# Kernel tuning notes

Measured on AMD Instinct MI355X. Metric: run time of the kernel, lower is better.

## Reference

```python
import jax, jax.numpy as jnp
from jax import lax
import numpy as np

P = 32      # num_series
H = 128     # hidden units
B = 32      # batch
T = 256     # sequence length

def setup_inputs() -> dict:
    key = jax.random.key(0)
    ks = jax.random.split(key, 8)
    s = 1.0 / np.sqrt(H)
    X     = jax.random.normal(ks[0], (B, T, P), dtype=jnp.float32)
    # per-network LSTM weights, PyTorch gate order (i, f, g, o) stacked in 4H
    W_ih  = jax.random.uniform(ks[1], (P, 4 * H, P), dtype=jnp.float32, minval=-s, maxval=s)
    W_hh  = jax.random.uniform(ks[2], (P, 4 * H, H), dtype=jnp.float32, minval=-s, maxval=s)
    b_ih  = jax.random.uniform(ks[3], (P, 4 * H), dtype=jnp.float32, minval=-s, maxval=s)
    b_hh  = jax.random.uniform(ks[4], (P, 4 * H), dtype=jnp.float32, minval=-s, maxval=s)
    # Conv1d(hidden, 1, kernel_size=1) == per-timestep linear H -> 1, per network
    W_out = jax.random.uniform(ks[5], (P, H), dtype=jnp.float32, minval=-s, maxval=s)
    b_out = jax.random.uniform(ks[6], (P,), dtype=jnp.float32, minval=-s, maxval=s)
    return {"X": X, "W_ih": W_ih, "W_hh": W_hh, "b_ih": b_ih,
            "b_hh": b_hh, "W_out": W_out, "b_out": b_out}

def reference(X, W_ih, W_hh, b_ih, b_hh, W_out, b_out):
    # X: (B, T, P); p independent 1-layer LSTMs run on the same input,
    # batched along a network axis n (size P) with distinct weights.
    # Precompute input projections for all steps/networks: (T, B, P, 4H)
    xproj = jnp.einsum('btd,nkd->tbnk', X, W_ih) + b_ih + b_hh

    def step(carry, xp_t):
        h, c = carry                                   # (B, P, H) each
        gates = xp_t + jnp.einsum('bnh,nkh->bnk', h, W_hh)
        i, f, g, o = jnp.split(gates, 4, axis=-1)
        i = jax.nn.sigmoid(i)
        f = jax.nn.sigmoid(f)
        g = jnp.tanh(g)
        o = jax.nn.sigmoid(o)
        c = f * c + i * g
        h = o * jnp.tanh(c)
        return (h, c), h

    h0 = jnp.zeros((X.shape[0], W_ih.shape[0], W_hh.shape[2]), X.dtype)
    (_, _), hs = lax.scan(step, (h0, h0), xproj)        # hs: (T, B, P, H)
    # 1x1 conv head per network, then concat over networks -> (B, T, P)
    pred = jnp.einsum('tbnh,nh->btn', hs, W_out) + b_out
    return pred
```

## Files before the change

kernel.cpp:

```cpp
#include <hip/hip_runtime.h>
#include <stdint.h>

#define NP 32
#define NH 128
#define NB 32
#define NT 256
#define FH 512

typedef __attribute__((ext_vector_type(4))) float float4_t;
typedef __attribute__((ext_vector_type(8))) __bf16 bf16x8;
typedef __attribute__((ext_vector_type(4))) __bf16 bf16x4;

static __device__ __forceinline__ float4_t mfma_bf16(bf16x8 a, bf16x8 b, float4_t c) {
  return __builtin_amdgcn_mfma_f32_16x16x32_bf16(a, b, c, 0, 0, 0);
}

#define LOG2E 1.4426950408889634f

#define BAR() __asm__ volatile("s_waitcnt lgkmcnt(0)\n\ts_barrier" ::: "memory")


__global__ __launch_bounds__(512, 1) void xcvt(
    const float* __restrict__ X, __bf16* __restrict__ Xb)
{
  const int i = (blockIdx.x * 512 + threadIdx.x) * 4;
  float4_t v = *(const float4_t*)(X + i);
  bf16x4 o;
#pragma unroll
  for (int j = 0; j < 4; ++j) o[j] = (__bf16)v[j];
  *(bf16x4*)(Xb + i) = o;
}

__global__ __attribute__((amdgpu_flat_work_group_size(512, 512),
                          amdgpu_waves_per_eu(2, 2)))
void clstm_fused7(
    const __bf16* __restrict__ Xb, const float* __restrict__ Wih,
    const float* __restrict__ Whh, const float* __restrict__ bih,
    const float* __restrict__ bhh, const float* __restrict__ Wout,
    const float* __restrict__ bout, float* __restrict__ out)
{
  const int net = blockIdx.x & 31, bq = blockIdx.x >> 5;
  const int tid = threadIdx.x;
  const int w = tid >> 6, lane = tid & 63;
  const int quad = lane >> 4, l16 = lane & 15;

  __shared__ __bf16 hfrag[2][4][4][4][8];

  { ((int*)hfrag)[tid] = 0; }
  __syncthreads();

  bf16x8 bfrag[4][5];
  float4_t bias4[4];
#pragma unroll
  for (int g = 0; g < 4; ++g) {
    const float scale = (g == 2) ? (-2.0f*LOG2E) : (-LOG2E);
    const int col = g*NH + w*16 + l16;
#pragma unroll
    for (int kc = 0; kc < 5; ++kc) {
      const float* src = (kc == 0) ? (Wih + ((size_t)net*FH + col)*NP + quad*8)
                                   : (Whh + ((size_t)net*FH + col)*NH + (kc-1)*32 + quad*8);
      bf16x8 bf;
#pragma unroll
      for (int j = 0; j < 8; ++j) bf[j] = (__bf16)(src[j] * scale);
      bfrag[g][kc] = bf;
    }
    const float b = (bih[net*FH + col] + bhh[net*FH + col]) * scale;
    bias4[g] = (float4_t){b, b, b, b};
  }

  bf16x8 wof[4];
#pragma unroll
  for (int kc = 0; kc < 4; ++kc) {
    const float* wp = Wout + net*NH + kc*32 + quad*8;
#pragma unroll
    for (int j = 0; j < 8; ++j) wof[kc][j] = (__bf16)wp[j];
  }
  const float bo = bout[net];

  float cs = 0.f;
  const float S2 = -2.0f*LOG2E;

  int xoff = (bq*4 + (l16 >> 2))*(NT*NP) + quad*8;

  const int kcp = w >> 1, q2 = ((w & 1) << 1) | (l16 >> 3), jj = l16 & 7;

  float* outp = out + ((size_t)(bq*4 + quad))*(NT*NP) + net;

  bf16x8 ax = *(const bf16x8*)(Xb + xoff);
  xoff += NP;

#define STEP(RD, WR, T_)                                                      \
  do {                                                                        \
                 \
    bf16x8 ah0 = *(const bf16x8*)&hfrag[RD][0][quad][l16 >> 2][0];            \
    bf16x8 ah1 = *(const bf16x8*)&hfrag[RD][1][quad][l16 >> 2][0];            \
    bf16x8 ah2 = *(const bf16x8*)&hfrag[RD][2][quad][l16 >> 2][0];            \
    bf16x8 ah3 = *(const bf16x8*)&hfrag[RD][3][quad][l16 >> 2][0];            \
        \
    float4_t a0 = mfma_bf16(ax, bfrag[0][0], bias4[0]);                       \
    float4_t a1 = mfma_bf16(ax, bfrag[1][0], bias4[1]);                       \
    float4_t a2 = mfma_bf16(ax, bfrag[2][0], bias4[2]);                       \
    float4_t a3 = mfma_bf16(ax, bfrag[3][0], bias4[3]);                       \
               \
    if ((T_) + 1 < NT)                                                        \
      ax = *(const bf16x8*)(Xb + xoff);                                       \
    xoff += NP;                                                               \
                       \
    a0 = mfma_bf16(ah0, bfrag[0][1], a0);                                     \
    a1 = mfma_bf16(ah0, bfrag[1][1], a1);                                     \
    a2 = mfma_bf16(ah0, bfrag[2][1], a2);                                     \
    a3 = mfma_bf16(ah0, bfrag[3][1], a3);                                     \
    a0 = mfma_bf16(ah1, bfrag[0][2], a0);                                     \
    a1 = mfma_bf16(ah1, bfrag[1][2], a1);                                     \
    a2 = mfma_bf16(ah1, bfrag[2][2], a2);                                     \
    a3 = mfma_bf16(ah1, bfrag[3][2], a3);                                     \
    a0 = mfma_bf16(ah2, bfrag[0][3], a0);                                     \
    a1 = mfma_bf16(ah2, bfrag[1][3], a1);                                     \
    a2 = mfma_bf16(ah2, bfrag[2][3], a2);                                     \
    a3 = mfma_bf16(ah2, bfrag[3][3], a3);                                     \
    a0 = mfma_bf16(ah3, bfrag[0][4], a0);                                     \
    a1 = mfma_bf16(ah3, bfrag[1][4], a1);                                     \
    a2 = mfma_bf16(ah3, bfrag[2][4], a2);                                     \
    a3 = mfma_bf16(ah3, bfrag[3][4], a3);                                     \
                \
    float ei = __builtin_amdgcn_exp2f(a0[0]);                                 \
    float ig = __builtin_amdgcn_rcpf(1.0f + ei);              \
    float ef = __builtin_amdgcn_exp2f(a1[0]);                                 \
    float fg = __builtin_amdgcn_rcpf(1.0f + ef);              \
    float eg = __builtin_amdgcn_exp2f(fminf(a2[0], 126.0f));                  \
    float rg = __builtin_amdgcn_rcpf(1.0f + eg);                              \
    float t0 = S2 * rg;                                                       \
    float gg2 = t0 - t0 * eg;                                 \
    float eo = __builtin_amdgcn_exp2f(a3[0]);                                 \
    float og = __builtin_amdgcn_rcpf(1.0f + eo);              \
    cs = fg * cs + ig * gg2;                                      \
    float ec = __builtin_amdgcn_exp2f(fminf(cs, 126.0f));                     \
    float rc = __builtin_amdgcn_rcpf(1.0f + ec);                              \
    float h_ = og * (rc - ec * rc);                            \
                       \
    hfrag[WR][kcp][q2][quad][jj] = (__bf16)h_;                                \
          \
    if ((T_) > 0 && w == ((T_) & 7)) {                                        \
      float4_t p0 = {bo, bo, bo, bo};                                         \
      float4_t p1 = {0.f, 0.f, 0.f, 0.f};                                     \
      p0 = mfma_bf16(ah0, wof[0], p0);                                        \
      p1 = mfma_bf16(ah2, wof[2], p1);                                        \
      p0 = mfma_bf16(ah1, wof[1], p0);                                        \
      p1 = mfma_bf16(ah3, wof[3], p1);                                        \
      if (l16 == 0)                                                           \
        outp[(size_t)((T_) - 1)*NP] = p0[0] + p1[0];                          \
    }                                                                         \
    BAR();                                                                    \
  } while (0)

  for (int t = 0; t < NT; t += 2) {
    STEP(0, 1, t);
    STEP(1, 0, t + 1);
  }
#undef STEP

  if (w == 0) {
    bf16x8 ahf[4];
#pragma unroll
    for (int kc = 0; kc < 4; ++kc)
      ahf[kc] = *(const bf16x8*)&hfrag[NT & 1][kc][quad][l16 >> 2][0];
    float4_t p0 = {bo, bo, bo, bo};
    float4_t p1 = {0.f, 0.f, 0.f, 0.f};
    p0 = mfma_bf16(ahf[0], wof[0], p0);
    p1 = mfma_bf16(ahf[2], wof[2], p1);
    p0 = mfma_bf16(ahf[1], wof[1], p0);
    p1 = mfma_bf16(ahf[3], wof[3], p1);
    if (l16 == 0)
      outp[(size_t)(NT - 1)*NP] = p0[0] + p1[0];
  }
}

__global__ __launch_bounds__(512, 1) void clstm_fused_fb(
    const float* __restrict__ X, const float* __restrict__ Wih,
    const float* __restrict__ Whh, const float* __restrict__ bih,
    const float* __restrict__ bhh, const float* __restrict__ Wout,
    const float* __restrict__ bout, float* __restrict__ out)
{
  const int net = blockIdx.x >> 3, bq = blockIdx.x & 7;
  const int tid = threadIdx.x;
  const int w = tid >> 6, lane = tid & 63;
  const int quad = lane >> 4, l16 = lane & 15;

  __shared__ __bf16 hfrag[2][4][4][4][8];
  { ((int*)hfrag)[tid] = 0; }
  __syncthreads();

  bf16x8 bfrag[4][5];
  float4_t bias4[4];
#pragma unroll
  for (int g = 0; g < 4; ++g) {
    const float scale = (g == 2) ? (-2.0f*LOG2E) : (-LOG2E);
    const int col = g*NH + w*16 + l16;
#pragma unroll
    for (int kc = 0; kc < 5; ++kc) {
      const float* src = (kc == 0) ? (Wih + ((size_t)net*FH + col)*NP + quad*8)
                                   : (Whh + ((size_t)net*FH + col)*NH + (kc-1)*32 + quad*8);
      bf16x8 bf;
#pragma unroll
      for (int j = 0; j < 8; ++j) bf[j] = (__bf16)(src[j] * scale);
      bfrag[g][kc] = bf;
    }
    const float b = (bih[net*FH + col] + bhh[net*FH + col]) * scale;
    bias4[g] = (float4_t){b, b, b, b};
  }

  bf16x8 wof[4];
#pragma unroll
  for (int kc = 0; kc < 4; ++kc) {
    const float* wp = Wout + net*NH + kc*32 + quad*8;
#pragma unroll
    for (int j = 0; j < 8; ++j) wof[kc][j] = (__bf16)wp[j];
  }
  const float bo = bout[net];

  float cs = 0.f;
  const float S2 = -2.0f*LOG2E;

  const float* xrow = X + (size_t)(bq*4 + (l16 & 3))*(NT*NP) + quad*8;
  const int kcp = w >> 1, q2 = ((w & 1) << 1) | (l16 >> 3), jj = l16 & 7;
  float* outp = out + ((size_t)bq*4)*(NT*NP) + net;

  bf16x8 ax;
  {
    float xv0[8];
    *(float4_t*)&xv0[0] = *(const float4_t*)xrow;
    *(float4_t*)&xv0[4] = *(const float4_t*)(xrow + 4);
#pragma unroll
    for (int j = 0; j < 8; ++j) ax[j] = (__bf16)xv0[j];
  }
  const float* xp = xrow + NP;
  float xv[8] = {0.f,0.f,0.f,0.f,0.f,0.f,0.f,0.f};

  for (int t = 0; t < NT; ++t) {
    const int rd = t & 1, wr = rd ^ 1;
    bf16x8 ah[4];
#pragma unroll
    for (int kc = 0; kc < 4; ++kc)
      ah[kc] = *(const bf16x8*)&hfrag[rd][kc][quad][l16 & 3][0];
    float4_t accx[4];
#pragma unroll
    for (int g = 0; g < 4; ++g)
      accx[g] = mfma_bf16(ax, bfrag[g][0], bias4[g]);
    if (t + 1 < NT) {
      *(float4_t*)&xv[0] = *(const float4_t*)xp;
      *(float4_t*)&xv[4] = *(const float4_t*)(xp + 4);
    }
    float4_t acc[4];
#pragma unroll
    for (int g = 0; g < 4; ++g) {
      float4_t a0 = mfma_bf16(ah[0], bfrag[g][1], accx[g]);
      float4_t a1 = mfma_bf16(ah[2], bfrag[g][3], (float4_t){0.f,0.f,0.f,0.f});
      a0 = mfma_bf16(ah[1], bfrag[g][2], a0);
      a1 = mfma_bf16(ah[3], bfrag[g][4], a1);
      acc[g] = a0 + a1;
    }
    float gv[4];
#pragma unroll
    for (int g = 0; g < 4; ++g) {
      float a01 = (quad & 1) ? acc[g][1] : acc[g][0];
      float a23 = (quad & 1) ? acc[g][3] : acc[g][2];
      gv[g] = (quad & 2) ? a23 : a01;
    }
    float h;
    {
      float ei = __builtin_amdgcn_exp2f(gv[0]);
      float ig = __builtin_amdgcn_rcpf(1.0f + ei);
      float ef = __builtin_amdgcn_exp2f(gv[1]);
      float fg = __builtin_amdgcn_rcpf(1.0f + ef);
      float eg = __builtin_amdgcn_exp2f(fminf(gv[2], 126.0f));
      float rg = __builtin_amdgcn_rcpf(1.0f + eg);
      float t0 = S2 * rg;
      float gg2 = t0 - t0 * eg;
      float eo = __builtin_amdgcn_exp2f(gv[3]);
      float og = __builtin_amdgcn_rcpf(1.0f + eo);
      cs = fg * cs + ig * gg2;
      float ec = __builtin_amdgcn_exp2f(fminf(cs, 126.0f));
      float rc = __builtin_amdgcn_rcpf(1.0f + ec);
      float th = rc - ec * rc;
      h = og * th;
    }
    hfrag[wr][kcp][q2][quad][jj] = (__bf16)h;
    if (w == 0 && t > 0) {
      float4_t p0 = {bo, bo, bo, bo};
      float4_t p1 = {0.f, 0.f, 0.f, 0.f};
      p0 = mfma_bf16(ah[0], wof[0], p0);
      p1 = mfma_bf16(ah[2], wof[2], p1);
      p0 = mfma_bf16(ah[1], wof[1], p0);
      p1 = mfma_bf16(ah[3], wof[3], p1);
      float4_t po = p0 + p1;
      if (lane == 0) {
#pragma unroll
        for (int r = 0; r < 4; ++r)
          outp[(size_t)r*(NT*NP) + (t - 1)*NP] = po[r];
      }
    }
#pragma unroll
    for (int j = 0; j < 8; ++j) ax[j] = (__bf16)xv[j];
    xp += NP;
    BAR();
  }

  if (w == 0) {
    bf16x8 ahf[4];
#pragma unroll
    for (int kc = 0; kc < 4; ++kc)
      ahf[kc] = *(const bf16x8*)&hfrag[NT & 1][kc][quad][l16 & 3][0];
    float4_t p0 = {bo, bo, bo, bo};
    float4_t p1 = {0.f, 0.f, 0.f, 0.f};
    p0 = mfma_bf16(ahf[0], wof[0], p0);
    p1 = mfma_bf16(ahf[2], wof[2], p1);
    p0 = mfma_bf16(ahf[1], wof[1], p0);
    p1 = mfma_bf16(ahf[3], wof[3], p1);
    float4_t po = p0 + p1;
    if (lane == 0) {
#pragma unroll
      for (int r = 0; r < 4; ++r)
        outp[(size_t)r*(NT*NP) + (NT - 1)*NP] = po[r];
    }
  }
}

extern "C" void kernel_launch(void* const* d_in, const int* in_sizes, int n_in,
                              void* d_out, int out_size, void* d_ws, size_t ws_size,
                              hipStream_t stream) {
  const float* X    = (const float*)d_in[0];
  const float* Wih  = (const float*)d_in[1];
  const float* Whh  = (const float*)d_in[2];
  const float* bih  = (const float*)d_in[3];
  const float* bhh  = (const float*)d_in[4];
  const float* Wout = (const float*)d_in[5];
  const float* bout = (const float*)d_in[6];
  float* out = (float*)d_out;
  (void)in_sizes; (void)n_in; (void)out_size;

  const size_t need = (size_t)NB*NT*NP*2;
  if (d_ws != nullptr && ws_size >= need) {
    __bf16* wsX = (__bf16*)d_ws;
    xcvt<<<128, 512, 0, stream>>>(X, wsX);
    clstm_fused7<<<256, 512, 0, stream>>>(wsX, Wih, Whh, bih, bhh, Wout,
                                          bout, out);
  } else {
    clstm_fused_fb<<<256, 512, 0, stream>>>(X, Wih, Whh, bih, bhh, Wout,
                                            bout, out);
  }
}
```

Baseline: 207.2 us.

## Defer output projection: spill hidden states to workspace, project after recurrence

The per-step output head (four MFMAs plus a global store on one rotating wave) is removed from the serial recurrence loop. Each step instead writes its bf16 hidden state to a per-block workspace, and after the loop all threads compute the 1x1 conv head from global memory using Wout staged in LDS. The aim is to shorten the latency-bound critical path of each timestep. In exchange it adds about 67 MB of global writes and a read-back pass, needs a larger workspace, and falls back to the old path if the workspace is too small.

```diff
diff --git a/kernel.cpp b/kernel.cpp
--- a/kernel.cpp
+++ b/kernel.cpp
@@ -33,11 +33,12 @@
 
 __global__ __attribute__((amdgpu_flat_work_group_size(512, 512),
                           amdgpu_waves_per_eu(2, 2)))
-void clstm_fused7(
+void clstm_fused9(
     const __bf16* __restrict__ Xb, const float* __restrict__ Wih,
     const float* __restrict__ Whh, const float* __restrict__ bih,
     const float* __restrict__ bhh, const float* __restrict__ Wout,
-    const float* __restrict__ bout, float* __restrict__ out)
+    const float* __restrict__ bout, float* __restrict__ out,
+    __bf16* __restrict__ wsH)
 {
   const int net = blockIdx.x & 31, bq = blockIdx.x >> 5;
   const int tid = threadIdx.x;
@@ -68,15 +69,6 @@
     bias4[g] = (float4_t){b, b, b, b};
   }
 
-  bf16x8 wof[4];
-#pragma unroll
-  for (int kc = 0; kc < 4; ++kc) {
-    const float* wp = Wout + net*NH + kc*32 + quad*8;
-#pragma unroll
-    for (int j = 0; j < 8; ++j) wof[kc][j] = (__bf16)wp[j];
-  }
-  const float bo = bout[net];
-
   float cs = 0.f;
   const float S2 = -2.0f*LOG2E;
 
@@ -84,7 +76,8 @@
 
   const int kcp = w >> 1, q2 = ((w & 1) << 1) | (l16 >> 3), jj = l16 & 7;
 
-  float* outp = out + ((size_t)(bq*4 + quad))*(NT*NP) + net;
+  __bf16* wsHb = wsH + (size_t)blockIdx.x * (NT * 4 * NH);
+  int hoff = quad * NH + w * 16 + l16;
 
   bf16x8 ax = *(const bf16x8*)(Xb + xoff);
   xoff += NP;
@@ -137,19 +130,11 @@
     float ec = __builtin_amdgcn_exp2f(fminf(cs, 126.0f));                     \
     float rc = __builtin_amdgcn_rcpf(1.0f + ec);                              \
     float h_ = og * (rc - ec * rc);                            \
-                       \
+      \
+           \
     hfrag[WR][kcp][q2][quad][jj] = (__bf16)h_;                                \
-          \
-    if ((T_) > 0 && w == ((T_) & 7)) {                                        \
-      float4_t p0 = {bo, bo, bo, bo};                                         \
-      float4_t p1 = {0.f, 0.f, 0.f, 0.f};                                     \
-      p0 = mfma_bf16(ah0, wof[0], p0);                                        \
-      p1 = mfma_bf16(ah2, wof[2], p1);                                        \
-      p0 = mfma_bf16(ah1, wof[1], p0);                                        \
-      p1 = mfma_bf16(ah3, wof[3], p1);                                        \
-      if (l16 == 0)                                                           \
-        outp[(size_t)((T_) - 1)*NP] = p0[0] + p1[0];                          \
-    }                                                                         \
+    wsHb[hoff] = (__bf16)h_;                                                  \
+    hoff += 4 * NH;                                                           \
     BAR();                                                                    \
   } while (0)
 
@@ -159,19 +144,28 @@
   }
 #undef STEP
 
-  if (w == 0) {
-    bf16x8 ahf[4];
-#pragma unroll
-    for (int kc = 0; kc < 4; ++kc)
-      ahf[kc] = *(const bf16x8*)&hfrag[NT & 1][kc][quad][l16 >> 2][0];
-    float4_t p0 = {bo, bo, bo, bo};
-    float4_t p1 = {0.f, 0.f, 0.f, 0.f};
-    p0 = mfma_bf16(ahf[0], wof[0], p0);
-    p1 = mfma_bf16(ahf[2], wof[2], p1);
-    p0 = mfma_bf16(ahf[1], wof[1], p0);
-    p1 = mfma_bf16(ahf[3], wof[3], p1);
-    if (l16 == 0)
-      outp[(size_t)(NT - 1)*NP] = p0[0] + p1[0];
+  __asm__ volatile("s_waitcnt vmcnt(0)" ::: "memory");
+  __threadfence();
+  __syncthreads();
+  float* ldsW = (float*)&hfrag[0][0][0][0][0];
+  if (tid < NH) ldsW[tid] = Wout[net*NH + tid];
+  __syncthreads();
+
+  const float bo = bout[net];
+#pragma unroll
+  for (int rep = 0; rep < 2; ++rep) {
+    const int idx = tid + rep * 512;
+    const int tt = idx >> 2, b = idx & 3;
+    const __bf16* hp = wsHb + tt * (4 * NH) + b * NH;
+    float s = bo;
+#pragma unroll
+    for (int kc = 0; kc < 16; ++kc) {
+      bf16x8 h8 = *(const bf16x8*)(hp + kc * 8);
+#pragma unroll
+      for (int j = 0; j < 8; ++j)
+        s += (float)h8[j] * ldsW[kc * 8 + j];
+    }
+    out[(size_t)(bq * 4 + b) * (NT * NP) + tt * NP + net] = s;
   }
 }
 
@@ -338,12 +332,15 @@
   float* out = (float*)d_out;
   (void)in_sizes; (void)n_in; (void)out_size;
 
-  const size_t need = (size_t)NB*NT*NP*2;
+  const size_t nx = (size_t)NB * NT * NP;
+  const size_t nh = (size_t)256 * NT * 4 * NH;
+  const size_t need = (nx + nh) * sizeof(__bf16);
   if (d_ws != nullptr && ws_size >= need) {
     __bf16* wsX = (__bf16*)d_ws;
+    __bf16* wsH = wsX + nx;
     xcvt<<<128, 512, 0, stream>>>(X, wsX);
-    clstm_fused7<<<256, 512, 0, stream>>>(wsX, Wih, Whh, bih, bhh, Wout,
-                                          bout, out);
+    clstm_fused9<<<256, 512, 0, stream>>>(wsX, Wih, Whh, bih, bhh, Wout,
+                                          bout, out, wsH);
   } else {
     clstm_fused_fb<<<256, 512, 0, stream>>>(X, Wih, Whh, bih, bhh, Wout,
                                             bout, out);
```

Measured after the change: 243.7 us. +17.6%, slower.
